# Optimization experiments

Measured on AMD Instinct MI355X. Metric: run time of the kernel, lower is better.

The kernel has to match this reference:

```python
import jax, jax.numpy as jnp
import numpy as np

EMBED_DIM = 1024
NUM_HEADS = 16
HEAD_DIM = EMBED_DIM // NUM_HEADS
B, T = 2, 2048


def setup_inputs() -> dict:
    key = jax.random.key(0)
    ks = jax.random.split(key, 10)
    s_in = 1.0 / np.sqrt(EMBED_DIM)
    s_hd = 1.0 / np.sqrt(HEAD_DIM)
    return {
        "hidden_states": jax.random.normal(ks[0], (B, T, EMBED_DIM), jnp.float32),
        "attn_mask": jnp.zeros((T, T), jnp.float32),
        # per-head parameter stacks (nn.Linear: y = x @ W^T + b); store W pre-transposed
        "W_q": jax.random.uniform(ks[1], (NUM_HEADS, EMBED_DIM, HEAD_DIM), jnp.float32, -s_in, s_in),
        "b_q": jax.random.uniform(ks[2], (NUM_HEADS, HEAD_DIM), jnp.float32, -s_in, s_in),
        "W_k": jax.random.uniform(ks[3], (NUM_HEADS, EMBED_DIM, HEAD_DIM), jnp.float32, -s_in, s_in),
        "b_k": jax.random.uniform(ks[4], (NUM_HEADS, HEAD_DIM), jnp.float32, -s_in, s_in),
        "W_v": jax.random.uniform(ks[5], (NUM_HEADS, EMBED_DIM, HEAD_DIM), jnp.float32, -s_in, s_in),
        "b_v": jax.random.uniform(ks[6], (NUM_HEADS, HEAD_DIM), jnp.float32, -s_in, s_in),
        "W_o": jax.random.uniform(ks[7], (NUM_HEADS, HEAD_DIM, EMBED_DIM), jnp.float32, -s_hd, s_hd),
        "b_o": jax.random.uniform(ks[8], (NUM_HEADS, EMBED_DIM), jnp.float32, -s_hd, s_hd),
        "gate": jnp.ones((NUM_HEADS,), jnp.float32),
    }


def reference(hidden_states, attn_mask, W_q, b_q, W_k, b_k, W_v, b_v, W_o, b_o, gate):
    # All heads: state='active', consent=True (defaults); dropout in eval mode.
    scale = 1.0 / np.sqrt(HEAD_DIM)
    # Q,K,V: [B,H,T,hd]
    Q = jnp.einsum("btd,hde->bhte", hidden_states, W_q) + b_q[None, :, None, :]
    K = jnp.einsum("btd,hde->bhte", hidden_states, W_k) + b_k[None, :, None, :]
    V = jnp.einsum("btd,hde->bhte", hidden_states, W_v) + b_v[None, :, None, :]
    scores = jnp.einsum("bhte,bhse->bhts", Q, K) * scale + attn_mask[None, None, :, :]
    weights = jax.nn.softmax(scores, axis=-1)
    out = jnp.einsum("bhts,bhse->bhte", weights, V)  # [B,H,T,hd]
    # per-head scalar norm: mean over (B,T) of L2 norm along head_dim, floored at 1e-5
    denom = jnp.maximum(
        jnp.sqrt(jnp.sum(out * out, axis=-1)).mean(axis=(0, 2)), 1e-5
    )  # [H]
    out_n = out / denom[None, :, None, None]
    g = jnp.clip(gate, 0.0, 1.0)  # gate_factor = 1.0 for 'active' heads
    # projected per head: (out_n @ W_o + b_o) * g; then sum over heads / H
    proj = (jnp.einsum("bhte,hed->bhtd", out_n, W_o) + b_o[None, :, None, :]) * g[None, :, None, None]
    return proj.sum(axis=1) / NUM_HEADS
```

## Files before the change

### kernel.cpp

```cpp
#include <hip/hip_runtime.h>
#include <hip/hip_bf16.h>
#include <math.h>

#define EMBED_DIM 1024
#define NUM_HEADS 16
#define HEAD_DIM  64
#define B_SZ      2
#define T_SZ      2048
#define BT        (B_SZ * T_SZ)
#define LOG2E     1.44269504088896340736f
#define QSCALE    (0.125f * LOG2E)
#define SOFT_OFF  8.0f

typedef short bf16x8 __attribute__((ext_vector_type(8)));
typedef float f32x4  __attribute__((ext_vector_type(4)));

#define MFMA16(a, b, c) __builtin_amdgcn_mfma_f32_16x16x32_bf16((a), (b), (c), 0, 0, 0)

__device__ inline short f2bf(float f) {
    unsigned u = __builtin_bit_cast(unsigned, f);
    u = (u + 0x7fffu + ((u >> 16) & 1u)) >> 16;
    return (short)u;
}
__device__ inline float bf2f(short s) {
    unsigned u = ((unsigned)(unsigned short)s) << 16;
    return __builtin_bit_cast(float, u);
}
__device__ inline unsigned pk2(float a, float b) {
#if __has_builtin(__builtin_amdgcn_cvt_pk_bf16_f32)
    typedef __bf16 bf2_t __attribute__((ext_vector_type(2)));
    bf2_t t = __builtin_amdgcn_cvt_pk_bf16_f32(a, b);
    return __builtin_bit_cast(unsigned, t);
#else
    return (unsigned)(unsigned short)f2bf(a) | ((unsigned)(unsigned short)f2bf(b) << 16);
#endif
}

__device__ inline float ex2(float x) {
#if __has_builtin(__builtin_amdgcn_exp2f)
    return __builtin_amdgcn_exp2f(x);
#else
    return exp2f(x);
#endif
}

__device__ inline void gld16(const short* g, short* lds) {
    __builtin_amdgcn_global_load_lds(
        (const __attribute__((address_space(1))) void*)g,
        (__attribute__((address_space(3))) void*)lds, 16, 0, 0);
}

__device__ inline bf16x8 frag_swz(const short* tile, int R, int C) {
    return *(const bf16x8*)(tile + R * 64 + ((C ^ (R & 7)) << 3));
}

__device__ inline float red_add64(float v) {
    v += __shfl_xor(v, 1); v += __shfl_xor(v, 2); v += __shfl_xor(v, 4);
    v += __shfl_xor(v, 8); v += __shfl_xor(v, 16); v += __shfl_xor(v, 32);
    return v;
}

__global__ __launch_bounds__(256) void cvt_in_kernel(
    const float* __restrict__ hs, short* __restrict__ hsb)
{
    const long i = ((long)blockIdx.x * 256 + threadIdx.x) * 4;
    const float4 v = *(const float4*)(hs + i);
    ushort4 o; o.x = f2bf(v.x); o.y = f2bf(v.y); o.z = f2bf(v.z); o.w = f2bf(v.w);
    *(ushort4*)(hsb + i) = o;
}

__global__ __launch_bounds__(256) void mask_scan_kernel(
    const float* __restrict__ maskf, unsigned* __restrict__ flagsW)
{
    const int qc = blockIdx.x, kt = blockIdx.y;
    const float* base = maskf + (long)qc * 128 * 2048 + kt * 64;
    unsigned u = 0;
    const int tid = threadIdx.x;
    #pragma unroll
    for (int i = 0; i < 8; ++i) {
        const int flat = i * 256 + tid;
        const int r = flat >> 4, c4 = flat & 15;
        const uint4 v = *(const uint4*)(base + (long)r * 2048 + c4 * 4);
        u |= v.x | v.y | v.z | v.w;
    }
    if (__any(u != 0) && (tid & 63) == 0)
        atomicOr(&flagsW[qc], 1u << kt);
}

__global__ __launch_bounds__(256) void transpose_w_kernel(
    const float* __restrict__ Wq, const float* __restrict__ Wk,
    const float* __restrict__ Wv, const float* __restrict__ Wo,
    short* __restrict__ Wqt, short* __restrict__ Wkt,
    short* __restrict__ Wvt, short* __restrict__ WoT)
{
    const int arr = blockIdx.z, h = blockIdx.y;
    const float* src; short* dst; int R, C;
    if (arr == 0)      { src = Wq; dst = Wqt; R = 1024; C = 64; }
    else if (arr == 1) { src = Wk; dst = Wkt; R = 1024; C = 64; }
    else if (arr == 2) { src = Wv; dst = Wvt; R = 1024; C = 64; }
    else               { src = Wo; dst = WoT; R = 64;   C = 1024; }
    src += (long)h * 65536; dst += (long)h * 65536;

    const int ct = C / 32;
    const int tr = blockIdx.x / ct, tc = blockIdx.x % ct;
    __shared__ float tile[32][33];
    const int tx = threadIdx.x & 31, ty = threadIdx.x >> 5;
    #pragma unroll
    for (int i = 0; i < 4; ++i) {
        const int r = ty + 8 * i;
        tile[r][tx] = src[(long)(tr * 32 + r) * C + tc * 32 + tx];
    }
    __syncthreads();
    #pragma unroll
    for (int i = 0; i < 4; ++i) {
        const int r = ty + 8 * i;
        dst[(long)(tc * 32 + r) * R + tr * 32 + tx] = f2bf(tile[tx][r]);
    }
}

__global__ __launch_bounds__(256) void qkv_mfma_kernel(
    const short* __restrict__ hsb,
    const short* __restrict__ Wt,
    const float* __restrict__ bq, const float* __restrict__ bk,
    const float* __restrict__ bv,
    short* __restrict__ Qb, short* __restrict__ Kb, short* __restrict__ Vtb)
{
    const int m0 = blockIdx.x * 128;
    const int n0 = blockIdx.y * 128;
    __shared__ short As[128 * 64];
    __shared__ short Bs[128 * 64];

    const int tid = threadIdx.x, lane = tid & 63, w = tid >> 6;
    const int wm = w & 1, wn = w >> 1;
    const int quad = lane >> 4, l15 = lane & 15;

    f32x4 acc[4][4] = {};

    for (int k0 = 0; k0 < 1024; k0 += 64) {
        __syncthreads();
        #pragma unroll
        for (int t = 0; t < 4; ++t) {
            const int r0 = w * 32 + t * 8;
            const int r  = r0 + (lane >> 3);
            const int cg = (lane & 7) ^ (r & 7);
            gld16(hsb + (long)(m0 + r) * 1024 + k0 + cg * 8, &As[r0 * 64]);
            gld16(Wt  + (long)(n0 + r) * 1024 + k0 + cg * 8, &Bs[r0 * 64]);
        }
        __syncthreads();
        #pragma unroll
        for (int ks = 0; ks < 2; ++ks) {
            bf16x8 af[4];
            #pragma unroll
            for (int ms = 0; ms < 4; ++ms)
                af[ms] = frag_swz(As, wm * 64 + ms * 16 + l15, ks * 4 + quad);
            #pragma unroll
            for (int ns = 0; ns < 4; ++ns) {
                const bf16x8 bfr = frag_swz(Bs, wn * 64 + ns * 16 + l15, ks * 4 + quad);
                #pragma unroll
                for (int ms = 0; ms < 4; ++ms)
                    acc[ms][ns] = MFMA16(af[ms], bfr, acc[ms][ns]);
            }
        }
    }

    #pragma unroll
    for (int ns = 0; ns < 4; ++ns) {
        const int n    = n0 + wn * 64 + ns * 16 + l15;
        const int type = n >> 10;
        const int h    = (n >> 6) & 15;
        const int e    = n & 63;
        const float bias = (type == 0 ? bq : type == 1 ? bk : bv)[h * 64 + e];
        #pragma unroll
        for (int ms = 0; ms < 4; ++ms) {
            const int mbase = m0 + wm * 64 + ms * 16 + quad * 4;
            const int bb = mbase >> 11, t0 = mbase & 2047;
            if (type == 2) {
                const int tp = (t0 & ~63) | (t0 & 35) | ((t0 & 12) << 1) | ((t0 & 16) >> 2);
                ushort4 pk;
                pk.x = (unsigned short)f2bf(acc[ms][ns][0] + bias);
                pk.y = (unsigned short)f2bf(acc[ms][ns][1] + bias);
                pk.z = (unsigned short)f2bf(acc[ms][ns][2] + bias);
                pk.w = (unsigned short)f2bf(acc[ms][ns][3] + bias);
                *(ushort4*)&Vtb[((long)(bb * 16 + h) * 64 + e) * 2048 + tp] = pk;
            } else {
                #pragma unroll
                for (int r = 0; r < 4; ++r) {
                    const float v = acc[ms][ns][r] + bias;
                    const long off = ((long)(bb * 16 + h) * 2048 + (t0 + r)) * 64 + e;
                    if (type == 0) Qb[off] = f2bf(v * QSCALE);
                    else           Kb[off] = f2bf(v);
                }
            }
        }
    }
}

__global__ __launch_bounds__(512) void attn_mfma_kernel(
    const short* __restrict__ Qb, const short* __restrict__ Kb,
    const short* __restrict__ Vtb, const float* __restrict__ maskf,
    const unsigned* __restrict__ flagsW,
    short* __restrict__ Ob, float* __restrict__ denomsum)
{
    const int r_  = blockIdx.x;
    const int c_  = r_ & 7, j_ = r_ >> 3;
    const int g_  = c_ + 8 * (j_ >> 4);
    const int qc  = j_ & 15;
    const int q0  = qc * 128;
    const int h   = g_ & 15, b = g_ >> 4;
    const long bh = ((long)b * 16 + h) * (long)T_SZ * 64;

    __shared__ short Ks[2][64 * 64];
    __shared__ short Vs[2][64 * 64];
    __shared__ float wred[8];

    const int tid = threadIdx.x, lane = tid & 63, w = tid >> 6;
    const int quad = lane >> 4, l15 = lane & 15;
    const int qrow = q0 + w * 16 + l15;

    const unsigned zf = flagsW[qc];

    const short* Kg = Kb + bh;
    const short* Vg = Vtb + bh;

    bf16x8 qf[2];
    #pragma unroll
    for (int ks = 0; ks < 2; ++ks)
        qf[ks] = *(const bf16x8*)(Qb + bh + (long)qrow * 64 + ks * 32 + quad * 8);

    bf16x8 ones;
    #pragma unroll
    for (int i = 0; i < 8; ++i) ones[i] = (short)0x3F80;

    f32x4 o[4] = {};
    f32x4 lacc = {};

    const float* mrow = maskf + (long)qrow * 2048 + quad * 4;

    auto stageKV = [&](int kt, int buf) {
        const int kv0 = kt * 64;
        const int r0 = w * 8;
        const int r  = r0 + (lane >> 3);
        const int cg = (lane & 7) ^ (r & 7);
        gld16(Kg + (long)(kv0 + r) * 64 + cg * 8, &Ks[buf][r0 * 64]);
        gld16(Vg + (long)r * 2048 + kv0 + cg * 8, &Vs[buf][r0 * 64]);
    };

    stageKV(0, 0);

    for (int kt = 0; kt < 32; ++kt) {
        const int cur = kt & 1;

        __builtin_amdgcn_s_barrier();
        asm volatile("" ::: "memory");
        if (kt < 31) {
            stageKV(kt + 1, cur ^ 1);
            asm volatile("s_waitcnt vmcnt(2)" ::: "memory");
        } else {
            asm volatile("s_waitcnt vmcnt(0)" ::: "memory");
        }
        __builtin_amdgcn_s_barrier();
        asm volatile("" ::: "memory");

        f32x4 s[4];
        if (zf & (1u << kt)) {
            const int kv0 = kt * 64;
            #pragma unroll
            for (int kb = 0; kb < 4; ++kb) {
                const float4 m = *(const float4*)(mrow + kv0 + kb * 16);
                s[kb][0] = fmaf(m.x, LOG2E, -SOFT_OFF);
                s[kb][1] = fmaf(m.y, LOG2E, -SOFT_OFF);
                s[kb][2] = fmaf(m.z, LOG2E, -SOFT_OFF);
                s[kb][3] = fmaf(m.w, LOG2E, -SOFT_OFF);
            }
        } else {
            #pragma unroll
            for (int kb = 0; kb < 4; ++kb) {
                s[kb][0] = -SOFT_OFF; s[kb][1] = -SOFT_OFF;
                s[kb][2] = -SOFT_OFF; s[kb][3] = -SOFT_OFF;
            }
        }

        #pragma unroll
        for (int ks = 0; ks < 2; ++ks)
            #pragma unroll
            for (int kb = 0; kb < 4; ++kb) {
                const bf16x8 kf = frag_swz(&Ks[cur][0], kb * 16 + l15, ks * 4 + quad);
                s[kb] = MFMA16(kf, qf[ks], s[kb]);
            }

        unsigned w0[4], w1[4];
        #pragma unroll
        for (int kb = 0; kb < 4; ++kb) {
            const float p0 = ex2(s[kb][0]);
            const float p1 = ex2(s[kb][1]);
            const float p2 = ex2(s[kb][2]);
            const float p3 = ex2(s[kb][3]);
            w0[kb] = pk2(p0, p1);
            w1[kb] = pk2(p2, p3);
        }

        #pragma unroll
        for (int kbp = 0; kbp < 2; ++kbp) {
            const uint4 u = {w0[2 * kbp], w1[2 * kbp], w0[2 * kbp + 1], w1[2 * kbp + 1]};
            const bf16x8 pb = __builtin_bit_cast(bf16x8, u);
            lacc = MFMA16(ones, pb, lacc);
            #pragma unroll
            for (int eb = 0; eb < 4; ++eb) {
                const bf16x8 va = frag_swz(&Vs[cur][0], eb * 16 + l15, kbp * 4 + quad);
                o[eb] = MFMA16(va, pb, o[eb]);
            }
        }
    }

    const float inv = 1.f / lacc[0];
    float ss = 0.f;
    #pragma unroll
    for (int eb = 0; eb < 4; ++eb) {
        o[eb] *= inv;
        #pragma unroll
        for (int r = 0; r < 4; ++r) ss += o[eb][r] * o[eb][r];
    }
    ss += __shfl_xor(ss, 16);
    ss += __shfl_xor(ss, 32);
    const float tot = sqrtf(ss);

    #pragma unroll
    for (int eb = 0; eb < 4; ++eb) {
        uint2 pk;
        pk.x = pk2(o[eb][0], o[eb][1]);
        pk.y = pk2(o[eb][2], o[eb][3]);
        *(uint2*)&Ob[((long)(b * 2048 + qrow)) * 1024 + h * 64 + eb * 16 + quad * 4] = pk;
    }

    const float wsum = red_add64(tot) * 0.25f;
    if (lane == 0) wred[w] = wsum;
    __syncthreads();
    if (tid == 0) {
        float acc = 0.f;
        #pragma unroll
        for (int i = 0; i < 8; ++i) acc += wred[i];
        atomicAdd(&denomsum[h], acc);
    }
}

__global__ __launch_bounds__(256) void scale_w_kernel(
    short* __restrict__ WoT, const float* __restrict__ denomsum,
    const float* __restrict__ gate)
{
    __shared__ float sh[16];
    if (threadIdx.x < 16) {
        const float g  = fminf(fmaxf(gate[threadIdx.x], 0.f), 1.f);
        const float dn = fmaxf(denomsum[threadIdx.x] * (1.f / (float)BT), 1e-5f);
        sh[threadIdx.x] = g / (dn * (float)NUM_HEADS);
    }
    __syncthreads();
    const long i = ((long)blockIdx.x * 256 + threadIdx.x) * 4;
    const float sc = sh[(int)(i >> 16)];
    ushort4 v = *(ushort4*)(WoT + i);
    v.x = (unsigned short)f2bf(bf2f((short)v.x) * sc);
    v.y = (unsigned short)f2bf(bf2f((short)v.y) * sc);
    v.z = (unsigned short)f2bf(bf2f((short)v.z) * sc);
    v.w = (unsigned short)f2bf(bf2f((short)v.w) * sc);
    *(ushort4*)(WoT + i) = v;
}

__global__ __launch_bounds__(256) void oproj_mfma_kernel(
    const short* __restrict__ Ob,
    const short* __restrict__ WoT,
    const float* __restrict__ bo,
    const float* __restrict__ gate,
    float* __restrict__ out)
{
    const int m0 = blockIdx.x * 64;
    const int n0 = blockIdx.y * 128;
    __shared__ short As[2][64 * 64];
    __shared__ short Bs[2][128 * 64];

    const int tid = threadIdx.x, lane = tid & 63, w = tid >> 6;
    const int wm = w & 1, wn = w >> 1;
    const int quad = lane >> 4, l15 = lane & 15;

    auto stage = [&](int h, int buf) {
        #pragma unroll
        for (int t = 0; t < 2; ++t) {
            const int r0 = w * 16 + t * 8;
            const int r  = r0 + (lane >> 3);
            const int cg = (lane & 7) ^ (r & 7);
            gld16(Ob + (long)(m0 + r) * 1024 + h * 64 + cg * 8, &As[buf][r0 * 64]);
        }
        #pragma unroll
        for (int t = 0; t < 4; ++t) {
            const int r0 = w * 32 + t * 8;
            const int r  = r0 + (lane >> 3);
            const int cg = (lane & 7) ^ (r & 7);
            gld16(WoT + (long)h * 65536 + (long)(n0 + r) * 64 + cg * 8, &Bs[buf][r0 * 64]);
        }
    };

    f32x4 acc[2][4] = {};
    stage(0, 0);

    for (int h = 0; h < 16; ++h) {
        const int cur = h & 1;
        __syncthreads();
        if (h < 15) stage(h + 1, cur ^ 1);
        #pragma unroll
        for (int ks = 0; ks < 2; ++ks) {
            bf16x8 af[2];
            #pragma unroll
            for (int ms = 0; ms < 2; ++ms)
                af[ms] = frag_swz(&As[cur][0], wm * 32 + ms * 16 + l15, ks * 4 + quad);
            #pragma unroll
            for (int ns = 0; ns < 4; ++ns) {
                const bf16x8 bfr = frag_swz(&Bs[cur][0], wn * 64 + ns * 16 + l15, ks * 4 + quad);
                #pragma unroll
                for (int ms = 0; ms < 2; ++ms)
                    acc[ms][ns] = MFMA16(af[ms], bfr, acc[ms][ns]);
            }
        }
    }

    float gcl[16];
    #pragma unroll
    for (int hh = 0; hh < 16; ++hh)
        gcl[hh] = fminf(fmaxf(gate[hh], 0.f), 1.f) * (1.f / (float)NUM_HEADS);

    #pragma unroll
    for (int ns = 0; ns < 4; ++ns) {
        const int n = n0 + wn * 64 + ns * 16 + l15;
        float be = 0.f;
        #pragma unroll
        for (int hh = 0; hh < 16; ++hh) be += gcl[hh] * bo[hh * 1024 + n];
        #pragma unroll
        for (int ms = 0; ms < 2; ++ms) {
            const int m = m0 + wm * 32 + ms * 16 + quad * 4;
            #pragma unroll
            for (int r = 0; r < 4; ++r)
                out[(long)(m + r) * 1024 + n] = acc[ms][ns][r] + be;
        }
    }
}

extern "C" void kernel_launch(void* const* d_in, const int* in_sizes, int n_in,
                              void* d_out, int out_size, void* d_ws, size_t ws_size,
                              hipStream_t stream)
{
    const float* hs   = (const float*)d_in[0];
    const float* mask = (const float*)d_in[1];
    const float* Wq   = (const float*)d_in[2];
    const float* bq   = (const float*)d_in[3];
    const float* Wk   = (const float*)d_in[4];
    const float* bk   = (const float*)d_in[5];
    const float* Wv   = (const float*)d_in[6];
    const float* bv   = (const float*)d_in[7];
    const float* Wo   = (const float*)d_in[8];
    const float* bo   = (const float*)d_in[9];
    const float* gate = (const float*)d_in[10];
    float* out = (float*)d_out;

    char* ws = (char*)d_ws;
    const size_t MB = 1024 * 1024;
    short* hsb   = (short*)(ws);
    short* Wqt   = (short*)(ws + 8  * MB);
    short* Wkt   = (short*)(ws + 10 * MB);
    short* Wvt   = (short*)(ws + 12 * MB);
    short* WoT   = (short*)(ws + 14 * MB);
    short* Qb    = (short*)(ws + 16 * MB);
    short* Kb    = (short*)(ws + 24 * MB);
    short* Vtb   = (short*)(ws + 32 * MB);
    short* Ob    = (short*)(ws + 40 * MB);
    float* denomsum = (float*)(ws + 48 * MB);
    unsigned* flagsW = (unsigned*)(ws + 48 * MB + 4096);

    (void)hipMemsetAsync(denomsum, 0, NUM_HEADS * sizeof(float), stream);
    (void)hipMemsetAsync(flagsW, 0, 16 * sizeof(unsigned), stream);

    cvt_in_kernel<<<4096, 256, 0, stream>>>(hs, hsb);
    mask_scan_kernel<<<dim3(16, 32), 256, 0, stream>>>(mask, flagsW);
    transpose_w_kernel<<<dim3(64, 16, 4), 256, 0, stream>>>(
        Wq, Wk, Wv, Wo, Wqt, Wkt, Wvt, WoT);
    qkv_mfma_kernel<<<dim3(32, 24), 256, 0, stream>>>(
        hsb, Wqt, bq, bk, bv, Qb, Kb, Vtb);
    attn_mfma_kernel<<<512, 512, 0, stream>>>(
        Qb, Kb, Vtb, mask, flagsW, Ob, denomsum);
    scale_w_kernel<<<1024, 256, 0, stream>>>(WoT, denomsum, gate);
    oproj_mfma_kernel<<<dim3(64, 8), 256, 0, stream>>>(
        Ob, WoT, bo, gate, out);
}
```

Before: 225.4 us.

## Merge prep kernels, remap QKV grid for XCD locality, double attention KV tile

Three separate changes. The input conversion, mask scan and weight transpose kernels become one prep kernel that dispatches on block index, removing two launches. The QKV GEMM grid is flattened and remapped so that blocks landing on the same XCD share A and B tiles in L2. The attention kernel stages 128 KV rows per pipeline step instead of 64, halving the number of barrier and wait rounds at the cost of twice the LDS (64 KB per block), which may lower occupancy.

```diff
diff --git a/kernel.cpp b/kernel.cpp
--- a/kernel.cpp
+++ b/kernel.cpp
@@ -60,61 +60,61 @@
     return v;
 }
 
-__global__ __launch_bounds__(256) void cvt_in_kernel(
-    const float* __restrict__ hs, short* __restrict__ hsb)
-{
-    const long i = ((long)blockIdx.x * 256 + threadIdx.x) * 4;
-    const float4 v = *(const float4*)(hs + i);
-    ushort4 o; o.x = f2bf(v.x); o.y = f2bf(v.y); o.z = f2bf(v.z); o.w = f2bf(v.w);
-    *(ushort4*)(hsb + i) = o;
-}
-
-__global__ __launch_bounds__(256) void mask_scan_kernel(
-    const float* __restrict__ maskf, unsigned* __restrict__ flagsW)
-{
-    const int qc = blockIdx.x, kt = blockIdx.y;
-    const float* base = maskf + (long)qc * 128 * 2048 + kt * 64;
-    unsigned u = 0;
-    const int tid = threadIdx.x;
-    #pragma unroll
-    for (int i = 0; i < 8; ++i) {
-        const int flat = i * 256 + tid;
-        const int r = flat >> 4, c4 = flat & 15;
-        const uint4 v = *(const uint4*)(base + (long)r * 2048 + c4 * 4);
-        u |= v.x | v.y | v.z | v.w;
-    }
-    if (__any(u != 0) && (tid & 63) == 0)
-        atomicOr(&flagsW[qc], 1u << kt);
-}
-
-__global__ __launch_bounds__(256) void transpose_w_kernel(
+__global__ __launch_bounds__(256) void prep_kernel(
+    const float* __restrict__ hs, short* __restrict__ hsb,
+    const float* __restrict__ maskf, unsigned* __restrict__ flagsW,
     const float* __restrict__ Wq, const float* __restrict__ Wk,
     const float* __restrict__ Wv, const float* __restrict__ Wo,
     short* __restrict__ Wqt, short* __restrict__ Wkt,
     short* __restrict__ Wvt, short* __restrict__ WoT)
 {
-    const int arr = blockIdx.z, h = blockIdx.y;
-    const float* src; short* dst; int R, C;
-    if (arr == 0)      { src = Wq; dst = Wqt; R = 1024; C = 64; }
-    else if (arr == 1) { src = Wk; dst = Wkt; R = 1024; C = 64; }
-    else if (arr == 2) { src = Wv; dst = Wvt; R = 1024; C = 64; }
-    else               { src = Wo; dst = WoT; R = 64;   C = 1024; }
-    src += (long)h * 65536; dst += (long)h * 65536;
-
-    const int ct = C / 32;
-    const int tr = blockIdx.x / ct, tc = blockIdx.x % ct;
     __shared__ float tile[32][33];
-    const int tx = threadIdx.x & 31, ty = threadIdx.x >> 5;
-    #pragma unroll
-    for (int i = 0; i < 4; ++i) {
-        const int r = ty + 8 * i;
-        tile[r][tx] = src[(long)(tr * 32 + r) * C + tc * 32 + tx];
-    }
-    __syncthreads();
-    #pragma unroll
-    for (int i = 0; i < 4; ++i) {
-        const int r = ty + 8 * i;
-        dst[(long)(tc * 32 + r) * R + tr * 32 + tx] = f2bf(tile[tx][r]);
+    const int bx = blockIdx.x, tid = threadIdx.x;
+
+    if (bx < 4096) {
+        const long i = ((long)bx * 256 + tid) * 4;
+        const float4 v = *(const float4*)(hs + i);
+        ushort4 o; o.x = f2bf(v.x); o.y = f2bf(v.y); o.z = f2bf(v.z); o.w = f2bf(v.w);
+        *(ushort4*)(hsb + i) = o;
+    } else if (bx < 4608) {
+        const int flat = bx - 4096;
+        const int qc = flat >> 5, kt = flat & 31;
+        const float* base = maskf + (long)qc * 128 * 2048 + kt * 64;
+        unsigned u = 0;
+        #pragma unroll
+        for (int i = 0; i < 8; ++i) {
+            const int f2 = i * 256 + tid;
+            const int r = f2 >> 4, c4 = f2 & 15;
+            const uint4 v = *(const uint4*)(base + (long)r * 2048 + c4 * 4);
+            u |= v.x | v.y | v.z | v.w;
+        }
+        if (__any(u != 0) && (tid & 63) == 0)
+            atomicOr(&flagsW[qc], 1u << kt);
+    } else {
+        const int j = bx - 4608;
+        const int x = j & 63, rest = j >> 6;
+        const int h = rest & 15, arr = rest >> 4;
+        const float* src; short* dst; int R, C;
+        if (arr == 0)      { src = Wq; dst = Wqt; R = 1024; C = 64; }
+        else if (arr == 1) { src = Wk; dst = Wkt; R = 1024; C = 64; }
+        else if (arr == 2) { src = Wv; dst = Wvt; R = 1024; C = 64; }
+        else               { src = Wo; dst = WoT; R = 64;   C = 1024; }
+        src += (long)h * 65536; dst += (long)h * 65536;
+
+        const int ct = C / 32;
+        const int tr = x / ct, tc = x % ct;
+        const int tx = tid & 31, ty = tid >> 5;
+        #pragma unroll
+        for (int i = 0; i < 4; ++i) {
+            const int r = ty + 8 * i;
+            tile[r][tx] = src[(long)(tr * 32 + r) * C + tc * 32 + tx];
+        }
+        __syncthreads();
+        #pragma unroll
+        for (int i = 0; i < 4; ++i) {
+            const int r = ty + 8 * i;
+            dst[(long)(tc * 32 + r) * R + tr * 32 + tx] = f2bf(tile[tx][r]);
+        }
     }
 }
 
@@ -125,8 +125,12 @@
     const float* __restrict__ bv,
     short* __restrict__ Qb, short* __restrict__ Kb, short* __restrict__ Vtb)
 {
-    const int m0 = blockIdx.x * 128;
-    const int n0 = blockIdx.y * 128;
+    const int r_ = blockIdx.x;
+    const int c_ = r_ & 7, j_ = r_ >> 3;
+    const int xi = j_ & 7, yi = j_ >> 3;
+    const int m0 = ((c_ & 3) * 8 + xi) * 128;
+    const int n0 = ((c_ >> 2) * 12 + yi) * 128;
+
     __shared__ short As[128 * 64];
     __shared__ short Bs[128 * 64];
 
@@ -209,8 +213,8 @@
     const int h   = g_ & 15, b = g_ >> 4;
     const long bh = ((long)b * 16 + h) * (long)T_SZ * 64;
 
-    __shared__ short Ks[2][64 * 64];
-    __shared__ short Vs[2][64 * 64];
+    __shared__ short Ks[2][128 * 64];
+    __shared__ short Vs[2][128 * 64];
     __shared__ float wred[8];
 
     const int tid = threadIdx.x, lane = tid & 63, w = tid >> 6;
@@ -236,78 +240,96 @@
 
     const float* mrow = maskf + (long)qrow * 2048 + quad * 4;
 
-    auto stageKV = [&](int kt, int buf) {
-        const int kv0 = kt * 64;
-        const int r0 = w * 8;
-        const int r  = r0 + (lane >> 3);
-        const int cg = (lane & 7) ^ (r & 7);
-        gld16(Kg + (long)(kv0 + r) * 64 + cg * 8, &Ks[buf][r0 * 64]);
-        gld16(Vg + (long)r * 2048 + kv0 + cg * 8, &Vs[buf][r0 * 64]);
+    auto stageKV = [&](int st, int buf) {
+        const int kv0 = st * 128;
+        #pragma unroll
+        for (int t = 0; t < 2; ++t) {
+            const int r0 = w * 16 + t * 8;
+            const int r  = r0 + (lane >> 3);
+            const int cg = (lane & 7) ^ (r & 7);
+            gld16(Kg + (long)(kv0 + r) * 64 + cg * 8, &Ks[buf][r0 * 64]);
+        }
+        #pragma unroll
+        for (int t = 0; t < 2; ++t) {
+            const int r0 = w * 8;
+            const int r  = r0 + (lane >> 3);
+            const int cg = (lane & 7) ^ (r & 7);
+            gld16(Vg + (long)r * 2048 + kv0 + t * 64 + cg * 8,
+                  &Vs[buf][t * 4096 + r0 * 64]);
+        }
     };
 
     stageKV(0, 0);
 
-    for (int kt = 0; kt < 32; ++kt) {
-        const int cur = kt & 1;
+    for (int st = 0; st < 16; ++st) {
+        const int cur = st & 1;
 
         __builtin_amdgcn_s_barrier();
         asm volatile("" ::: "memory");
-        if (kt < 31) {
-            stageKV(kt + 1, cur ^ 1);
-            asm volatile("s_waitcnt vmcnt(2)" ::: "memory");
+        if (st < 15) {
+            stageKV(st + 1, cur ^ 1);
+            asm volatile("s_waitcnt vmcnt(4)" ::: "memory");
         } else {
             asm volatile("s_waitcnt vmcnt(0)" ::: "memory");
         }
         __builtin_amdgcn_s_barrier();
         asm volatile("" ::: "memory");
 
-        f32x4 s[4];
-        if (zf & (1u << kt)) {
-            const int kv0 = kt * 64;
+        #pragma unroll
+        for (int k2 = 0; k2 < 2; ++k2) {
+            const int kt = st * 2 + k2;
+            const short* Kt = &Ks[cur][k2 * 4096];
+            const short* Vt = &Vs[cur][k2 * 4096];
+
+            f32x4 s[4];
+            if (zf & (1u << kt)) {
+                const int kv0 = kt * 64;
+                #pragma unroll
+                for (int kb = 0; kb < 4; ++kb) {
+                    const float4 m = *(const float4*)(mrow + kv0 + kb * 16);
+                    s[kb][0] = fmaf(m.x, LOG2E, -SOFT_OFF);
+                    s[kb][1] = fmaf(m.y, LOG2E, -SOFT_OFF);
+                    s[kb][2] = fmaf(m.z, LOG2E, -SOFT_OFF);
+                    s[kb][3] = fmaf(m.w, LOG2E, -SOFT_OFF);
+                }
+            } else {
+                #pragma unroll
+                for (int kb = 0; kb < 4; ++kb) {
+                    s[kb][0] = -SOFT_OFF; s[kb][1] = -SOFT_OFF;
+                    s[kb][2] = -SOFT_OFF; s[kb][3] = -SOFT_OFF;
+                }
+            }
+
+            #pragma unroll
+            for (int ks = 0; ks < 2; ++ks)
+                #pragma unroll
+                for (int kb = 0; kb < 4; ++kb) {
+                    const bf16x8 kf = frag_swz(Kt, kb * 16 + l15, ks * 4 + quad);
+                    s[kb] = MFMA16(kf, qf[ks], s[kb]);
+                }
+
+            unsigned w0[4], w1[4];
             #pragma unroll
             for (int kb = 0; kb < 4; ++kb) {
-                const float4 m = *(const float4*)(mrow + kv0 + kb * 16);
-                s[kb][0] = fmaf(m.x, LOG2E, -SOFT_OFF);
-                s[kb][1] = fmaf(m.y, LOG2E, -SOFT_OFF);
-                s[kb][2] = fmaf(m.z, LOG2E, -SOFT_OFF);
-                s[kb][3] = fmaf(m.w, LOG2E, -SOFT_OFF);
+                const float p0 = ex2(s[kb][0]);
+                const float p1 = ex2(s[kb][1]);
+                const float p2 = ex2(s[kb][2]);
+                const float p3 = ex2(s[kb][3]);
+                w0[kb] = pk2(p0, p1);
+                w1[kb] = pk2(p2, p3);
             }
-        } else {
-            #pragma unroll
-            for (int kb = 0; kb < 4; ++kb) {
-                s[kb][0] = -SOFT_OFF; s[kb][1] = -SOFT_OFF;
-                s[kb][2] = -SOFT_OFF; s[kb][3] = -SOFT_OFF;
-            }
-        }
-
-        #pragma unroll
-        for (int ks = 0; ks < 2; ++ks)
-            #pragma unroll
-            for (int kb = 0; kb < 4; ++kb) {
-                const bf16x8 kf = frag_swz(&Ks[cur][0], kb * 16 + l15, ks * 4 + quad);
-                s[kb] = MFMA16(kf, qf[ks], s[kb]);
-            }
-
-        unsigned w0[4], w1[4];
-        #pragma unroll
-        for (int kb = 0; kb < 4; ++kb) {
-            const float p0 = ex2(s[kb][0]);
-            const float p1 = ex2(s[kb][1]);
-            const float p2 = ex2(s[kb][2]);
-            const float p3 = ex2(s[kb][3]);
-            w0[kb] = pk2(p0, p1);
-            w1[kb] = pk2(p2, p3);
-        }
-
-        #pragma unroll
-        for (int kbp = 0; kbp < 2; ++kbp) {
-            const uint4 u = {w0[2 * kbp], w1[2 * kbp], w0[2 * kbp + 1], w1[2 * kbp + 1]};
-            const bf16x8 pb = __builtin_bit_cast(bf16x8, u);
-            lacc = MFMA16(ones, pb, lacc);
-            #pragma unroll
-            for (int eb = 0; eb < 4; ++eb) {
-                const bf16x8 va = frag_swz(&Vs[cur][0], eb * 16 + l15, kbp * 4 + quad);
-                o[eb] = MFMA16(va, pb, o[eb]);
+
+            #pragma unroll
+            for (int kbp = 0; kbp < 2; ++kbp) {
+                const uint4 u = {w0[2 * kbp], w1[2 * kbp],
+                                 w0[2 * kbp + 1], w1[2 * kbp + 1]};
+                const bf16x8 pb = __builtin_bit_cast(bf16x8, u);
+                lacc = MFMA16(ones, pb, lacc);
+                #pragma unroll
+                for (int eb = 0; eb < 4; ++eb) {
+                    const bf16x8 va = frag_swz(Vt, eb * 16 + l15, kbp * 4 + quad);
+                    o[eb] = MFMA16(va, pb, o[eb]);
+                }
             }
         }
     }
@@ -475,11 +497,9 @@
     (void)hipMemsetAsync(denomsum, 0, NUM_HEADS * sizeof(float), stream);
     (void)hipMemsetAsync(flagsW, 0, 16 * sizeof(unsigned), stream);
 
-    cvt_in_kernel<<<4096, 256, 0, stream>>>(hs, hsb);
-    mask_scan_kernel<<<dim3(16, 32), 256, 0, stream>>>(mask, flagsW);
-    transpose_w_kernel<<<dim3(64, 16, 4), 256, 0, stream>>>(
-        Wq, Wk, Wv, Wo, Wqt, Wkt, Wvt, WoT);
-    qkv_mfma_kernel<<<dim3(32, 24), 256, 0, stream>>>(
+    prep_kernel<<<8704, 256, 0, stream>>>(
+        hs, hsb, mask, flagsW, Wq, Wk, Wv, Wo, Wqt, Wkt, Wvt, WoT);
+    qkv_mfma_kernel<<<768, 256, 0, stream>>>(
         hsb, Wqt, bq, bk, bv, Qb, Kb, Vtb);
     attn_mfma_kernel<<<512, 512, 0, stream>>>(
         Qb, Kb, Vtb, mask, flagsW, Ob, denomsum);
```

After: 227.6 us. Within noise of the previous version (+1.0%).
